# Optimization experiments

Measured on AMD Instinct MI355X. Metric: run time of the kernel, lower is better.

Reference implementation:

```python
import jax, jax.numpy as jnp
import numpy as np
from jax import lax

B, L = 4, 2048
D_MODEL, D_STATE, D_CONV, EXPAND = 1024, 16, 4, 2
D_INNER = EXPAND * D_MODEL          # 2048
DT_RANK = (D_MODEL + 15) // 16      # 64 (mamba_ssm 'auto')
EPS = 1e-5


def setup_inputs() -> dict:
    key = jax.random.key(0)
    ks = jax.random.split(key, 10)
    s = 0.02
    x = jax.random.normal(ks[0], (B, L, D_MODEL), dtype=jnp.float32)
    ln_w = jnp.ones((D_MODEL,), jnp.float32)
    ln_b = jnp.zeros((D_MODEL,), jnp.float32)
    W_in = jax.random.normal(ks[1], (2 * D_INNER, D_MODEL), jnp.float32) * s
    conv_w = jax.random.normal(ks[2], (D_INNER, 1, D_CONV), jnp.float32) * s
    conv_b = jnp.zeros((D_INNER,), jnp.float32)
    W_x = jax.random.normal(ks[3], (DT_RANK + 2 * D_STATE, D_INNER), jnp.float32) * s
    W_dt = jax.random.normal(ks[4], (D_INNER, DT_RANK), jnp.float32) * s
    b_dt = jax.random.uniform(ks[5], (D_INNER,), jnp.float32, -4.0, -2.0)  # softplus(b)~small dt
    A_log = jnp.log(jnp.tile(jnp.arange(1.0, D_STATE + 1.0, dtype=jnp.float32), (D_INNER, 1)))
    Dp = jnp.ones((D_INNER,), jnp.float32)
    W_out = jax.random.normal(ks[6], (D_MODEL, D_INNER), jnp.float32) * s
    return dict(x=x, ln_w=ln_w, ln_b=ln_b, W_in=W_in, conv_w=conv_w, conv_b=conv_b,
                W_x=W_x, W_dt=W_dt, b_dt=b_dt, A_log=A_log, Dp=Dp, W_out=W_out)


def _mamba_forward(x, ln_w, ln_b, W_in, conv_w, conv_b, W_x, W_dt, b_dt, A_log, Dp, W_out):
    # LayerNorm
    mu = jnp.mean(x, axis=-1, keepdims=True)
    var = jnp.mean(jnp.square(x - mu), axis=-1, keepdims=True)
    xn = (x - mu) * lax.rsqrt(var + EPS) * ln_w + ln_b

    # in_proj -> (x_in, z), each [B, L, D_INNER]
    xz = jnp.einsum('bld,ed->ble', xn, W_in)
    x_in, z = jnp.split(xz, 2, axis=-1)

    # depthwise causal conv1d over time + SiLU
    xt = jnp.transpose(x_in, (0, 2, 1))  # [B, D_INNER, L]
    xc = lax.conv_general_dilated(xt, conv_w, window_strides=(1,),
                                  padding=[(D_CONV - 1, 0)],
                                  feature_group_count=D_INNER)
    xc = jax.nn.silu(jnp.transpose(xc + conv_b[None, :, None], (0, 2, 1)))  # [B, L, D_INNER]

    # SSM parameterization
    x_dbl = jnp.einsum('bld,ed->ble', xc, W_x)  # [B, L, DT_RANK + 2*D_STATE]
    dt_r, Bs, Cs = jnp.split(x_dbl, [DT_RANK, DT_RANK + D_STATE], axis=-1)
    dt = jax.nn.softplus(jnp.einsum('blr,dr->bld', dt_r, W_dt) + b_dt)  # [B, L, D_INNER]
    A = -jnp.exp(A_log)  # [D_INNER, D_STATE]

    # selective scan over time (time-major)
    def step(h, inp):
        dt_t, B_t, C_t, u_t = inp  # [B,dI], [B,dS], [B,dS], [B,dI]
        dA = jnp.exp(dt_t[:, :, None] * A)                     # [B, dI, dS]
        h = dA * h + (dt_t * u_t)[:, :, None] * B_t[:, None, :]
        y = jnp.sum(h * C_t[:, None, :], axis=-1)              # [B, dI]
        return h, y

    h0 = jnp.zeros((B, D_INNER, D_STATE), x.dtype)
    xs = (jnp.swapaxes(dt, 0, 1), jnp.swapaxes(Bs, 0, 1),
          jnp.swapaxes(Cs, 0, 1), jnp.swapaxes(xc, 0, 1))
    _, ys = lax.scan(step, h0, xs)
    y = jnp.swapaxes(ys, 0, 1) + xc * Dp  # [B, L, D_INNER]

    # gate + out_proj + residual
    y = y * jax.nn.silu(z)
    out = jnp.einsum('ble,de->bld', y, W_out)
    return x + out


def reference(x, ln_w, ln_b, W_in, conv_w, conv_b, W_x, W_dt, b_dt, A_log, Dp, W_out):
    return _mamba_forward(x, ln_w, ln_b, W_in, conv_w, conv_b, W_x, W_dt, b_dt, A_log, Dp, W_out)
```

## Files before the change

kernel.cpp:

```cpp
#include <hip/hip_runtime.h>
#include <math.h>

#define BB 4
#define LL 2048
#define DM 1024
#define DI 2048
#define DS 16
#define DTR 64
#define TCH 256
#define TT 16

typedef unsigned short bf16;
typedef __attribute__((ext_vector_type(8))) short bf16x8;
typedef __attribute__((ext_vector_type(4))) float f32x4;
typedef __attribute__((ext_vector_type(2))) float f32x2;

__device__ inline float b2f(bf16 u) { return __uint_as_float(((unsigned)u) << 16); }
__device__ inline bf16 f2b(float f) {
    unsigned u = __float_as_uint(f);
    u += 0x7FFF + ((u >> 16) & 1);
    return (bf16)(u >> 16);
}

__device__ inline float4 ld4(const float* p) { return *(const float4*)p; }
__device__ inline float4 ld4(const bf16* p) {
    ushort4 v = *(const ushort4*)p;
    return make_float4(b2f(v.x), b2f(v.y), b2f(v.z), b2f(v.w));
}
__device__ inline void st1(float* p, float v) { *p = v; }
__device__ inline void st1(bf16* p, float v) { *p = f2b(v); }

__device__ inline float softplus_fast(float v) {
    return (v > 15.f) ? v : __logf(1.f + __expf(v));
}

__device__ inline void gld_lds16(const void* g, void* l) {
    __builtin_amdgcn_global_load_lds(
        (const __attribute__((address_space(1))) unsigned int*)g,
        (__attribute__((address_space(3))) unsigned int*)l, 16, 0, 0);
}

__device__ inline void dA2_tree(float c1, f32x2* dA2) {
    float c2 = c1 * c1;
    float c4 = c2 * c2;
    float c8 = c4 * c4;
    f32x2 c2v = {c2, c2};
    f32x2 c8v = {c8, c8};
    dA2[0] = (f32x2){c1, c2};
    dA2[1] = dA2[0] * c2v;
    dA2[2] = dA2[1] * c2v;
    dA2[3] = dA2[2] * c2v;
    dA2[4] = dA2[0] * c8v;
    dA2[5] = dA2[1] * c8v;
    dA2[6] = dA2[2] * c8v;
    dA2[7] = dA2[3] * c8v;
}

__global__ __launch_bounds__(256) void f2b_kernel(const float* __restrict__ in,
    bf16* __restrict__ out, int n4)
{
    int i = blockIdx.x * 256 + threadIdx.x;
    if (i >= n4) return;
    float4 v = *(const float4*)(in + (size_t)i * 4);
    ushort4 o = { f2b(v.x), f2b(v.y), f2b(v.z), f2b(v.w) };
    *(ushort4*)(out + (size_t)i * 4) = o;
}

__global__ __launch_bounds__(256) void prep_kernel(
    const float* __restrict__ x, const float* __restrict__ lw,
    const float* __restrict__ lb, bf16* __restrict__ xn,
    const float* __restrict__ W_in, bf16* __restrict__ W_in_b,
    const float* __restrict__ W_x, bf16* __restrict__ W_x_b,
    const float* __restrict__ W_dt, bf16* __restrict__ W_dt_b,
    const float* __restrict__ cw, bf16* __restrict__ cwt,
    const float* __restrict__ W_out, bf16* __restrict__ W_out_b,
    int dofast, int dowout)
{
    int blk = blockIdx.x;
    int tid = threadIdx.x;
    if (blk < BB * LL) {
        int row = blk;
        const float* xr = x + (size_t)row * DM;
        float4 v = *(const float4*)(xr + tid * 4);
        float s1 = v.x + v.y + v.z + v.w;
        float s2 = v.x * v.x + v.y * v.y + v.z * v.z + v.w * v.w;
        #pragma unroll
        for (int o = 32; o > 0; o >>= 1) {
            s1 += __shfl_xor(s1, o);
            s2 += __shfl_xor(s2, o);
        }
        __shared__ float r1[4], r2[4];
        __shared__ float smu, srs;
        int wv = tid >> 6;
        if ((tid & 63) == 0) { r1[wv] = s1; r2[wv] = s2; }
        __syncthreads();
        if (tid == 0) {
            float t1 = r1[0] + r1[1] + r1[2] + r1[3];
            float t2 = r2[0] + r2[1] + r2[2] + r2[3];
            float mu = t1 * (1.0f / DM);
            float var = t2 * (1.0f / DM) - mu * mu;
            smu = mu;
            srs = rsqrtf(var + 1e-5f);
        }
        __syncthreads();
        float mu = smu, rs = srs;
        float4 wv4 = *(const float4*)(lw + tid * 4);
        float4 bv4 = *(const float4*)(lb + tid * 4);
        ushort4 o;
        o.x = f2b((v.x - mu) * rs * wv4.x + bv4.x);
        o.y = f2b((v.y - mu) * rs * wv4.y + bv4.y);
        o.z = f2b((v.z - mu) * rs * wv4.z + bv4.z);
        o.w = f2b((v.w - mu) * rs * wv4.w + bv4.w);
        *(ushort4*)(xn + (size_t)row * DM + tid * 4) = o;
        return;
    }
    blk -= BB * LL;
    if (blk < 4096) {
        int i = blk * 256 + tid;
        float4 v = *(const float4*)(W_in + (size_t)i * 4);
        ushort4 o = { f2b(v.x), f2b(v.y), f2b(v.z), f2b(v.w) };
        *(ushort4*)(W_in_b + (size_t)i * 4) = o;
        return;
    }
    blk -= 4096;
    if (!dofast) return;
    if (blk < 192) {
        int i = blk * 256 + tid;
        float4 v = *(const float4*)(W_x + (size_t)i * 4);
        ushort4 o = { f2b(v.x), f2b(v.y), f2b(v.z), f2b(v.w) };
        *(ushort4*)(W_x_b + (size_t)i * 4) = o;
        return;
    }
    blk -= 192;
    if (blk < 128) {
        int i = blk * 256 + tid;
        float4 v = *(const float4*)(W_dt + (size_t)i * 4);
        ushort4 o = { f2b(v.x), f2b(v.y), f2b(v.z), f2b(v.w) };
        *(ushort4*)(W_dt_b + (size_t)i * 4) = o;
        return;
    }
    blk -= 128;
    if (blk < 8) {
        int d = blk * 256 + tid;
        float4 w = *(const float4*)(cw + d * 4);
        cwt[0 * DI + d] = f2b(w.x);
        cwt[1 * DI + d] = f2b(w.y);
        cwt[2 * DI + d] = f2b(w.z);
        cwt[3 * DI + d] = f2b(w.w);
        return;
    }
    blk -= 8;
    if (dowout && blk < 2048) {
        int i = blk * 256 + tid;
        float4 v = *(const float4*)(W_out + (size_t)i * 4);
        ushort4 o = { f2b(v.x), f2b(v.y), f2b(v.z), f2b(v.w) };
        *(ushort4*)(W_out_b + (size_t)i * 4) = o;
    }
}

#define BARR  do { asm volatile("" ::: "memory"); __builtin_amdgcn_s_barrier(); \
                   asm volatile("" ::: "memory"); } while (0)
#define LGKM0 do { asm volatile("s_waitcnt lgkmcnt(0)" ::: "memory"); \
                   __builtin_amdgcn_sched_barrier(0); } while (0)
#define VMC4  asm volatile("s_waitcnt vmcnt(4)" ::: "memory")
#define VMC2  asm volatile("s_waitcnt vmcnt(2)" ::: "memory")
#define SCHED0 __builtin_amdgcn_sched_barrier(0)

template<int EPI, typename TC>
__global__ __launch_bounds__(512, 2) void gemm_8p(
    const bf16* __restrict__ A, int lda,
    const bf16* __restrict__ B, int ldb,
    TC* __restrict__ C, int ldc,
    int K, const float* __restrict__ aux, int nbn)
{
    __shared__ bf16 lds[65536];
    char* L = (char*)lds;
    const int tid = threadIdx.x;
    const int lane = tid & 63;
    const int w = tid >> 6;
    const int wm = w >> 2;
    const int wn = w & 3;

    int nwg = gridDim.x;
    int bid = blockIdx.x;
    int sb = bid;
    if ((nwg & 7) == 0) sb = (bid & 7) * (nwg >> 3) + (bid >> 3);
    const int m0 = (sb / nbn) * 256;
    const int n0 = (sb % nbn) * 256;

    const size_t lda2 = (size_t)lda * 2;
    const size_t ldb2 = (size_t)ldb * 2;
    const int l8 = lane >> 3;
    const int scol = ((lane & 7) ^ l8) << 4;
    const size_t offA = (size_t)(w * 8 + l8) * lda2 + scol;
    const size_t offB = (size_t)(w * 8 + l8) * ldb2 + scol;
    const char* Ab = (const char*)A + (size_t)m0 * lda2;
    const char* Bb = (const char*)B + (size_t)n0 * ldb2;

    const int fm = lane & 15, fq = lane >> 4;
    const int prow = fm * 128;
    const int px0 = (fq << 4) ^ ((fm & 7) << 4);
    const int px1 = (64 | (fq << 4)) ^ ((fm & 7) << 4);
    const char* Lar = L + wm * 16384 + prow;
    const char* Lbr = L + 65536 + (wn >> 1) * 16384 + (wn & 1) * 8192 + prow;

    f32x4 acc[8][4] = {};
    bf16x8 a_[2][2], b_[4][2];

#define ST_A(sbuf, hh, t) do { \
    const char* s_ = Ab + (size_t)(hh) * 128 * lda2 + (size_t)(t) * 128 + offA; \
    gld_lds16(s_,             L + (sbuf) * 32768 + (hh) * 16384 + w * 1024); \
    gld_lds16(s_ + 64 * lda2, L + (sbuf) * 32768 + (hh) * 16384 + 8192 + w * 1024); \
  } while (0)
#define ST_B(sbuf, hh, t) do { \
    const char* s_ = Bb + (size_t)(hh) * 128 * ldb2 + (size_t)(t) * 128 + offB; \
    gld_lds16(s_,             L + 65536 + (sbuf) * 32768 + (hh) * 16384 + w * 1024); \
    gld_lds16(s_ + 64 * ldb2, L + 65536 + (sbuf) * 32768 + (hh) * 16384 + 8192 + w * 1024); \
  } while (0)
#define DS_A1(rb, q, kh) do { \
    a_[0][kh] = *(const bf16x8*)(Lar + (rb) * 32768 + ((q) * 32 +  0) * 128 + ((kh) ? px1 : px0)); \
    a_[1][kh] = *(const bf16x8*)(Lar + (rb) * 32768 + ((q) * 32 + 16) * 128 + ((kh) ? px1 : px0)); \
  } while (0)
#define DS_Bh(rb, kh) do { \
    _Pragma("unroll") \
    for (int ni = 0; ni < 4; ni++) \
      b_[ni][kh] = *(const bf16x8*)(Lbr + (rb) * 32768 + ni * 2048 + ((kh) ? px1 : px0)); \
  } while (0)
#define MFMA_H(q, kh) do { \
    _Pragma("unroll") \
    for (int mi = 0; mi < 2; mi++) \
      _Pragma("unroll") \
      for (int ni = 0; ni < 4; ni++) \
        acc[(q)*2+mi][ni] = __builtin_amdgcn_mfma_f32_16x16x32_bf16( \
            a_[mi][kh], b_[ni][kh], acc[(q)*2+mi][ni], 0, 0, 0); \
  } while (0)
#define PHASE(rb, q, rb2, q2, STAGE, DOVMC) do { \
    STAGE; \
    if (DOVMC) VMC4; \
    BARR; LGKM0; \
    __builtin_amdgcn_s_setprio(1); \
    MFMA_H(q, 0); \
    __builtin_amdgcn_s_setprio(0); \
    DS_A1(rb2, q2, 0); \
    if ((q) == 3) DS_Bh(rb2, 0); \
    SCHED0; \
    __builtin_amdgcn_s_setprio(1); \
    MFMA_H(q, 1); \
    __builtin_amdgcn_s_setprio(0); \
    DS_A1(rb2, q2, 1); \
    if ((q) == 3) DS_Bh(rb2, 1); \
    BARR; \
  } while (0)

    const int NT = K >> 6;
    ST_B(0, 0, 0); ST_B(0, 1, 0);
    ST_A(0, 0, 0); ST_A(0, 1, 0);
    ST_B(1, 0, 1); ST_B(1, 1, 1);
    VMC4;
    BARR;
    DS_Bh(0, 0); DS_Bh(0, 1);
    DS_A1(0, 0, 0); DS_A1(0, 0, 1);

    for (int t0 = 0; t0 < NT; t0 += 2) {
        const int tA1 = t0 + 1;
        const int tN2 = (t0 + 2 < NT) ? t0 + 2 : NT - 1;
        const int tN3 = (t0 + 3 < NT) ? t0 + 3 : NT - 1;
        PHASE(0, 0, 0, 1, ST_A(1, 0, tA1), 0);
        PHASE(0, 1, 0, 2, ST_A(1, 1, tA1), 0);
        PHASE(0, 2, 0, 3, ST_B(0, 0, tN2), 0);
        PHASE(0, 3, 1, 0, ST_B(0, 1, tN2), 1);
        PHASE(1, 0, 1, 1, ST_A(0, 0, tN2), 0);
        PHASE(1, 1, 1, 2, ST_A(0, 1, tN2), 0);
        PHASE(1, 2, 1, 3, ST_B(1, 0, tN3), 0);
        PHASE(1, 3, 0, 0, ST_B(1, 1, tN3), 1);
    }
    asm volatile("s_waitcnt vmcnt(0)" ::: "memory");

    #pragma unroll
    for (int i = 0; i < 8; i++) {
        #pragma unroll
        for (int ni = 0; ni < 4; ni++) {
            int n = n0 + wn * 64 + ni * 16 + fm;
            #pragma unroll
            for (int r = 0; r < 4; r++) {
                int m = m0 + wm * 128 + i * 16 + fq * 4 + r;
                float v = acc[i][ni][r];
                if (EPI == 2) v += aux[(size_t)m * ldc + n];
                st1(&C[(size_t)m * ldc + n], v);
            }
        }
    }
#undef ST_A
#undef ST_B
#undef DS_A1
#undef DS_Bh
#undef MFMA_H
#undef PHASE
}

template<int EPI, typename TC>
__global__ __launch_bounds__(512, 2) void gemm_8p_n128(
    const bf16* __restrict__ A, int lda,
    const bf16* __restrict__ B, int ldb,
    TC* __restrict__ C, int ldc,
    int K, const float* __restrict__ aux, int nbn)
{
    __shared__ bf16 lds[49152];
    char* L = (char*)lds;
    const int tid = threadIdx.x;
// ... 35 lines not shown
  } while (0)
#define ST_B1(sbuf, hh, t) do { \
    const char* s_ = Bb + (size_t)(hh) * 64 * ldb2 + (size_t)(t) * 128 + offB; \
    gld_lds16(s_, L + 65536 + (sbuf) * 16384 + (hh) * 8192 + w * 1024); \
  } while (0)
#define DS_A1h(rb, q, kh) do { \
    a_[kh] = *(const bf16x8*)(Lar + (rb) * 32768 + ((q) * 16) * 128 + ((kh) ? px1 : px0)); \
  } while (0)
#define DS_Bh(rb, kh) do { \
    _Pragma("unroll") \
    for (int ni = 0; ni < 4; ni++) \
      b_[ni][kh] = *(const bf16x8*)(Lbr + (rb) * 16384 + ni * 2048 + ((kh) ? px1 : px0)); \
  } while (0)
#define MFMA_Hh(q, kh) do { \
    _Pragma("unroll") \
    for (int ni = 0; ni < 4; ni++) \
      acc[q][ni] = __builtin_amdgcn_mfma_f32_16x16x32_bf16( \
          a_[kh], b_[ni][kh], acc[q][ni], 0, 0, 0); \
  } while (0)
#define PHASE(rb, q, rb2, q2, STAGE, DOVMC) do { \
    STAGE; \
    if (DOVMC) VMC2; \
    BARR; LGKM0; \
    __builtin_amdgcn_s_setprio(1); \
    MFMA_Hh(q, 0); \
    __builtin_amdgcn_s_setprio(0); \
    DS_A1h(rb2, q2, 0); \
    if ((q) == 3) DS_Bh(rb2, 0); \
    SCHED0; \
    __builtin_amdgcn_s_setprio(1); \
    MFMA_Hh(q, 1); \
    __builtin_amdgcn_s_setprio(0); \
    DS_A1h(rb2, q2, 1); \
    if ((q) == 3) DS_Bh(rb2, 1); \
    BARR; \
  } while (0)

    const int NT = K >> 6;
    ST_B1(0, 0, 0); ST_B1(0, 1, 0);
    ST_A(0, 0, 0); ST_A(0, 1, 0);
    ST_B1(1, 0, 1); ST_B1(1, 1, 1);
    VMC2;
    BARR;
    DS_Bh(0, 0); DS_Bh(0, 1);
    DS_A1h(0, 0, 0); DS_A1h(0, 0, 1);

    for (int t0 = 0; t0 < NT; t0 += 2) {
        const int tA1 = t0 + 1;
        const int tN2 = (t0 + 2 < NT) ? t0 + 2 : NT - 1;
        const int tN3 = (t0 + 3 < NT) ? t0 + 3 : NT - 1;
        PHASE(0, 0, 0, 1, ST_A(1, 0, tA1), 0);
        PHASE(0, 1, 0, 2, ST_A(1, 1, tA1), 0);
        PHASE(0, 2, 0, 3, ST_B1(0, 0, tN2), 0);
        PHASE(0, 3, 1, 0, ST_B1(0, 1, tN2), 1);
        PHASE(1, 0, 1, 1, ST_A(0, 0, tN2), 0);
        PHASE(1, 1, 1, 2, ST_A(0, 1, tN2), 0);
        PHASE(1, 2, 1, 3, ST_B1(1, 0, tN3), 0);
        PHASE(1, 3, 0, 0, ST_B1(1, 1, tN3), 1);
    }
    asm volatile("s_waitcnt vmcnt(0)" ::: "memory");

    #pragma unroll
    for (int i = 0; i < 4; i++) {
        #pragma unroll
        for (int ni = 0; ni < 4; ni++) {
            int n = n0 + wn * 64 + ni * 16 + fm;
            #pragma unroll
            for (int r = 0; r < 4; r++) {
                int m = m0 + wm * 64 + i * 16 + fq * 4 + r;
                float v = acc[i][ni][r];
                if (EPI == 2) v += aux[(size_t)m * ldc + n];
                st1(&C[(size_t)m * ldc + n], v);
            }
        }
    }
#undef ST_A
#undef ST_B1
#undef DS_A1h
#undef DS_Bh
#undef MFMA_Hh
#undef PHASE
}

template<int EPI, typename TC>
__global__ __launch_bounds__(256) void gemm_mfma(
    const bf16* __restrict__ A, int lda,
    const bf16* __restrict__ B, int ldb,
    TC* __restrict__ C, int ldc,
    int K, const float* __restrict__ aux)
{
    __shared__ bf16 As[128 * 32];
    __shared__ bf16 Bs[128 * 32];
    const int tid = threadIdx.x;
    const int lane = tid & 63;
    const int w = tid >> 6;
    const int wm = w >> 1, wn = w & 1;
    const int m0 = blockIdx.y * 128, n0 = blockIdx.x * 128;

    const int srow = lane >> 2;
    const int schunk = (lane & 3) * 8;

    const int fm = lane & 15;
    const int fq = lane >> 4;

    f32x4 acc[4][4] = {};

    for (int kt = 0; kt < K; kt += 32) {
        #pragma unroll
        for (int i = 0; i < 2; i++) {
            int r0 = i * 64 + w * 16;
            gld_lds16(A + (size_t)(m0 + r0 + srow) * lda + kt + schunk, &As[r0 * 32]);
            gld_lds16(B + (size_t)(n0 + r0 + srow) * ldb + kt + schunk, &Bs[r0 * 32]);
        }
        __syncthreads();
        bf16x8 af[4], bfr[4];
        #pragma unroll
        for (int i = 0; i < 4; i++) {
            af[i]  = *(const bf16x8*)&As[(wm * 64 + i * 16 + fm) * 32 + fq * 8];
            bfr[i] = *(const bf16x8*)&Bs[(wn * 64 + i * 16 + fm) * 32 + fq * 8];
        }
        #pragma unroll
        for (int i = 0; i < 4; i++)
            #pragma unroll
            for (int j = 0; j < 4; j++)
                acc[i][j] = __builtin_amdgcn_mfma_f32_16x16x32_bf16(
                    af[i], bfr[j], acc[i][j], 0, 0, 0);
        __syncthreads();
    }

    #pragma unroll
    for (int i = 0; i < 4; i++) {
        #pragma unroll
        for (int r = 0; r < 4; r++) {
            int m = m0 + wm * 64 + i * 16 + fq * 4 + r;
            #pragma unroll
            for (int j = 0; j < 4; j++) {
                int n = n0 + wn * 64 + j * 16 + fm;
                float v = acc[i][j][r];
                if (EPI == 1) {
                    v = softplus_fast(v + aux[n]);
                } else if (EPI == 2) {
                    v += aux[(size_t)m * ldc + n];
                }
                st1(&C[(size_t)m * ldc + n], v);
            }
        }
    }
}

__global__ __launch_bounds__(256) void xproj_mfma(
    const bf16* __restrict__ A,
    const bf16* __restrict__ Bm,
    float* __restrict__ Cx,
    bf16* __restrict__ dtr)
{
    __shared__ bf16 As[32 * 32];
    __shared__ bf16 Bs[128 * 32];
    const int tid = threadIdx.x;
    const int lane = tid & 63;
    const int w = tid >> 6;
    const int wm = w >> 1, wn = w & 1;
    const int m0 = blockIdx.x * 32;
    const int srow = lane >> 2;
    const int schunk = (lane & 3) * 8;
    const int fm = lane & 15;
    const int fq = lane >> 4;
    f32x4 acc[3] = {};
    for (int kt = 0; kt < DI; kt += 32) {
        if (w < 2) {
            int r0 = w * 16;
            gld_lds16(A + (size_t)(m0 + r0 + srow) * DI + kt + schunk, &As[r0 * 32]);
        }
        {
            int r0 = w * 32;
            gld_lds16(Bm + (size_t)(r0 + srow) * DI + kt + schunk, &Bs[r0 * 32]);
            gld_lds16(Bm + (size_t)(r0 + 16 + srow) * DI + kt + schunk, &Bs[(r0 + 16) * 32]);
        }
        __syncthreads();
        bf16x8 af = *(const bf16x8*)&As[(wm * 16 + fm) * 32 + fq * 8];
        #pragma unroll
        for (int j = 0; j < 3; j++) {
            bf16x8 bf = *(const bf16x8*)&Bs[((wn * 3 + j) * 16 + fm) * 32 + fq * 8];
            acc[j] = __builtin_amdgcn_mfma_f32_16x16x32_bf16(af, bf, acc[j], 0, 0, 0);
        }
        __syncthreads();
    }
    #pragma unroll
    for (int j = 0; j < 3; j++) {
        int col = (wn * 3 + j) * 16 + fm;
        #pragma unroll
        for (int r = 0; r < 4; r++) {
            int m = m0 + wm * 16 + fq * 4 + r;
            float v = acc[j][r];
            Cx[(size_t)m * 96 + col] = v;
            if (col < 64) dtr[(size_t)m * 64 + col] = f2b(v);
        }
    }
}

template<int EPI, typename TA, typename TB, typename TC>
__global__ __launch_bounds__(256) void gemm_nt(
    const TA* __restrict__ A, int lda,
    const TB* __restrict__ B, int ldb,
    TC* __restrict__ C, int ldc,
    int M, int N, int K,
    const float* __restrict__ aux)
{
    __shared__ float As[16][64];
    __shared__ float Bs[16][64];
    int tid = threadIdx.x;
    int m0 = blockIdx.y * 64, n0 = blockIdx.x * 64;
    int lr = tid >> 2;
    int lc = (tid & 3) * 4;
    int tm = tid >> 4;
    int tn = tid & 15;
    float acc[4][4] = {};
    for (int kt = 0; kt < K; kt += 16) {
        float4 av = ld4(A + (size_t)(m0 + lr) * lda + kt + lc);
        float4 bv = make_float4(0.f, 0.f, 0.f, 0.f);
        if (n0 + lr < N)
            bv = ld4(B + (size_t)(n0 + lr) * ldb + kt + lc);
        As[lc + 0][lr] = av.x; As[lc + 1][lr] = av.y;
        As[lc + 2][lr] = av.z; As[lc + 3][lr] = av.w;
        Bs[lc + 0][lr] = bv.x; Bs[lc + 1][lr] = bv.y;
        Bs[lc + 2][lr] = bv.z; Bs[lc + 3][lr] = bv.w;
        __syncthreads();
        #pragma unroll
        for (int k = 0; k < 16; k++) {
            float4 a4 = *(const float4*)&As[k][tm * 4];
            float4 b4 = *(const float4*)&Bs[k][tn * 4];
            float am[4] = {a4.x, a4.y, a4.z, a4.w};
            float bn[4] = {b4.x, b4.y, b4.z, b4.w};
            #pragma unroll
            for (int i = 0; i < 4; i++)
                #pragma unroll
                for (int j = 0; j < 4; j++)
                    acc[i][j] = fmaf(am[i], bn[j], acc[i][j]);
        }
        __syncthreads();
    }
    #pragma unroll
    for (int i = 0; i < 4; i++) {
        int m = m0 + tm * 4 + i;
        #pragma unroll
        for (int j = 0; j < 4; j++) {
            int n = n0 + tn * 4 + j;
            if (n >= N) continue;
            float v = acc[i][j];
            if (EPI == 1) {
                v = softplus_fast(v + aux[n]);
            }
            st1(&C[(size_t)m * ldc + n], v);
        }
    }
}

__global__ __launch_bounds__(256) void conv_silu_kernel(
    const bf16* __restrict__ xz, const bf16* __restrict__ cwt,
    const float* __restrict__ cb, bf16* __restrict__ xc)
{
    int idx = blockIdx.x * 256 + threadIdx.x;
    int d8 = idx & (DI / 8 - 1);
    int bl = idx >> 8;
    int l = bl & (LL - 1);
    int d0 = d8 * 8;
    float4 b0 = *(const float4*)(cb + d0);
    float4 b1 = *(const float4*)(cb + d0 + 4);
    float acc[8] = {b0.x, b0.y, b0.z, b0.w, b1.x, b1.y, b1.z, b1.w};
    #pragma unroll
    for (int k = 0; k < 4; k++) {
        if (l - 3 + k < 0) continue;
        bf16x8 xv = *(const bf16x8*)(xz + (size_t)(bl - 3 + k) * (2 * DI) + d0);
        bf16x8 wv = *(const bf16x8*)(cwt + k * DI + d0);
        #pragma unroll
        for (int j = 0; j < 8; j++)
            acc[j] = fmaf(b2f((bf16)xv[j]), b2f((bf16)wv[j]), acc[j]);
    }
    bf16x8 o;
    #pragma unroll
    for (int j = 0; j < 8; j++)
        o[j] = (short)f2b(acc[j] / (1.f + __expf(-acc[j])));
    *(bf16x8*)(xc + (size_t)bl * DI + d0) = o;
}

template<int NCC>
__global__ __launch_bounds__(256) void scan_part1(
    const float* __restrict__ xdbl, const bf16* __restrict__ dty,
    const bf16* __restrict__ xc, const float* __restrict__ A_log,
    float* __restrict__ Pd, float* __restrict__ S)
{
    __shared__ bf16 sdt[TT][TCH];
    __shared__ bf16 su[TT][TCH];
    __shared__ alignas(16) float sBC[TT][32];
    __shared__ int sflag;
    const int CH = LL / NCC;
    int bid = blockIdx.x;
    int cg = bid & 7;
    int c  = (bid >> 3) & (NCC - 1);
    int b  = (bid >> 3) / NCC;
    int d0 = cg * TCH;
    int tid = threadIdx.x;
    int w = tid >> 6, l = tid & 63;
    int lrow = l >> 5, lcol = (l & 31) * 8;
    int brow = l >> 3, bcol = (l & 7) * 4;
    int d = d0 + tid;

    if (tid == 0) sflag = 0;
    float Ads[16];
    #pragma unroll
    for (int q = 0; q < 4; q++) {
        float4 a4 = *(const float4*)&A_log[(size_t)d * DS + q * 4];
        Ads[q*4+0] = -__expf(a4.x); Ads[q*4+1] = -__expf(a4.y);
        Ads[q*4+2] = -__expf(a4.z); Ads[q*4+3] = -__expf(a4.w);
    }
    const float A0 = Ads[0];
    int bad = 0;
    #pragma unroll
    for (int s = 1; s < 16; s++) {
        float tgt = (float)(s + 1) * A0;
        bad |= (fabsf(Ads[s] - tgt) > 1e-5f * fabsf(tgt) + 1e-30f) ? 1 : 0;
    }
    __syncthreads();
    if (bad) atomicOr(&sflag, 1);
    __syncthreads();
    const int structured = (sflag == 0);

    const size_t rowbase = (size_t)b * LL + c * CH;
    float dsum = 0.f;

    if (structured) {
        f32x2 h2[8] = {};
        for (int t0 = 0; t0 < CH; t0 += TT) {
            #pragma unroll
            for (int pp = 0; pp < 2; pp++) {
                int r0 = (pp * 4 + w) * 2;
                size_t grow = rowbase + t0 + r0 + lrow;
                gld_lds16(dty + grow * DI + d0 + lcol, &sdt[r0][0]);
                gld_lds16(xc  + grow * DI + d0 + lcol, &su[r0][0]);
            }
            if (w < 2)
                gld_lds16(xdbl + (rowbase + t0 + w * 8 + brow) * 96 + DTR + bcol,
                          &sBC[w * 8][0]);
            __syncthreads();
            #pragma unroll
            for (int t = 0; t < TT; t++) {
                float dtv = b2f(sdt[t][tid]);
                float uv  = b2f(su[t][tid]);
                float tmp = dtv * uv;
                dsum += dtv;
                float4 B0 = ((const float4*)&sBC[t][0])[0];
                float4 B1 = ((const float4*)&sBC[t][0])[1];
                float4 B2 = ((const float4*)&sBC[t][0])[2];
                float4 B3 = ((const float4*)&sBC[t][0])[3];
                f32x2 bv2[8] = {{B0.x,B0.y},{B0.z,B0.w},{B1.x,B1.y},{B1.z,B1.w},
                                {B2.x,B2.y},{B2.z,B2.w},{B3.x,B3.y},{B3.z,B3.w}};
                f32x2 dA2[8];
                dA2_tree(__expf(dtv * A0), dA2);
                f32x2 tmp2 = {tmp, tmp};
                #pragma unroll
                for (int i = 0; i < 8; i++)
                    h2[i] = dA2[i] * h2[i] + tmp2 * bv2[i];
            }
            __syncthreads();
        }
        size_t o = ((size_t)(b * NCC + c) * DI + d) * DS;
        Pd[(size_t)(b * NCC + c) * DI + d] = dsum;
        #pragma unroll
        for (int q = 0; q < 4; q++)
            *(float4*)&S[o + q*4] = make_float4(h2[q*2].x, h2[q*2].y,
                                                h2[q*2+1].x, h2[q*2+1].y);
    } else {
        float h[16];
        #pragma unroll
        for (int s = 0; s < 16; s++) h[s] = 0.f;
        for (int t0 = 0; t0 < CH; t0 += TT) {
            #pragma unroll
            for (int pp = 0; pp < 2; pp++) {
                int r0 = (pp * 4 + w) * 2;
                size_t grow = rowbase + t0 + r0 + lrow;
                gld_lds16(dty + grow * DI + d0 + lcol, &sdt[r0][0]);
                gld_lds16(xc  + grow * DI + d0 + lcol, &su[r0][0]);
            }
            if (w < 2)
                gld_lds16(xdbl + (rowbase + t0 + w * 8 + brow) * 96 + DTR + bcol,
                          &sBC[w * 8][0]);
            __syncthreads();
            for (int t = 0; t < TT; t++) {
                float dtv = b2f(sdt[t][tid]);
                float uv  = b2f(su[t][tid]);
                float tmp = dtv * uv;
                dsum += dtv;
                const float4* bc = (const float4*)&sBC[t][0];
                float4 B0 = bc[0], B1 = bc[1], B2 = bc[2], B3 = bc[3];
                float Bv[16] = {B0.x,B0.y,B0.z,B0.w, B1.x,B1.y,B1.z,B1.w,
                                B2.x,B2.y,B2.z,B2.w, B3.x,B3.y,B3.z,B3.w};
                #pragma unroll
                for (int s = 0; s < 16; s++) {
                    float dA = __expf(dtv * Ads[s]);
                    h[s] = dA * h[s] + tmp * Bv[s];
                }
            }
            __syncthreads();
        }
        size_t o = ((size_t)(b * NCC + c) * DI + d) * DS;
        Pd[(size_t)(b * NCC + c) * DI + d] = dsum;
        #pragma unroll
        for (int q = 0; q < 4; q++)
            *(float4*)&S[o + q*4] = make_float4(h[q*4], h[q*4+1], h[q*4+2], h[q*4+3]);
    }
}

template<int NCC>
__global__ __launch_bounds__(256) void scan_combine(
    const float* __restrict__ A_log, const float* __restrict__ Pd,
    float* __restrict__ S)
{
    int g = blockIdx.x * 256 + threadIdx.x;
    int b = g >> 15;
    int rem = g & 32767;
    int d = rem >> 4;
    float Ads = -__expf(A_log[rem]);
    float h = 0.f;
    #pragma unroll
    for (int c = 0; c < NCC; c++) {
        size_t os = ((size_t)(b * NCC + c) << 15) + rem;
        float p = __expf(Ads * Pd[(size_t)(b * NCC + c) * DI + d]);
        float sv = S[os];
        S[os] = h;
        h = p * h + sv;
    }
}

template<int NCC>
__global__ __launch_bounds__(256) void scan_part2(
    const float* __restrict__ xdbl, bf16* __restrict__ dty,
    const bf16* __restrict__ xc, const bf16* __restrict__ xz,
    const float* __restrict__ A_log, const float* __restrict__ Dp,
    const float* __restrict__ Hin)
{
    __shared__ bf16 sdt[TT][TCH];
    __shared__ bf16 su[TT][TCH];
    __shared__ bf16 sz[TT][TCH];
    __shared__ alignas(16) float sBC[TT][32];
    __shared__ int sflag;
    const int CH = LL / NCC;
    int bid = blockIdx.x;
    int cg = bid & 7;
    int c  = (bid >> 3) & (NCC - 1);
    int b  = (bid >> 3) / NCC;
    int d0 = cg * TCH;
    int tid = threadIdx.x;
    int w = tid >> 6, l = tid & 63;
    int lrow = l >> 5, lcol = (l & 31) * 8;
    int brow = l >> 3, bcol = (l & 7) * 4;
    int d = d0 + tid;

    if (tid == 0) sflag = 0;
    float Ads[16];
    #pragma unroll
    for (int q = 0; q < 4; q++) {
        float4 a4 = *(const float4*)&A_log[(size_t)d * DS + q * 4];
        Ads[q*4+0] = -__expf(a4.x); Ads[q*4+1] = -__expf(a4.y);
        Ads[q*4+2] = -__expf(a4.z); Ads[q*4+3] = -__expf(a4.w);
    }
    const float A0 = Ads[0];
    int bad = 0;
    #pragma unroll
    for (int s = 1; s < 16; s++) {
        float tgt = (float)(s + 1) * A0;
        bad |= (fabsf(Ads[s] - tgt) > 1e-5f * fabsf(tgt) + 1e-30f) ? 1 : 0;
    }
    __syncthreads();
    if (bad) atomicOr(&sflag, 1);
    __syncthreads();
    const int structured = (sflag == 0);

    float dpd = Dp[d];
    size_t ho = ((size_t)(b * NCC + c) * DI + d) * DS;
    const size_t rowbase = (size_t)b * LL + c * CH;

    if (structured) {
        f32x2 h2[8];
        #pragma unroll
        for (int q = 0; q < 4; q++) {
            float4 hv = *(const float4*)&Hin[ho + q*4];
            h2[q*2]   = (f32x2){hv.x, hv.y};
            h2[q*2+1] = (f32x2){hv.z, hv.w};
        }
        for (int t0 = 0; t0 < CH; t0 += TT) {
            #pragma unroll
            for (int pp = 0; pp < 2; pp++) {
                int r0 = (pp * 4 + w) * 2;
                size_t grow = rowbase + t0 + r0 + lrow;
                gld_lds16(dty + grow * DI + d0 + lcol, &sdt[r0][0]);
                gld_lds16(xc  + grow * DI + d0 + lcol, &su[r0][0]);
                gld_lds16(xz  + grow * (2 * DI) + DI + d0 + lcol, &sz[r0][0]);
            }
            if (w < 2)
                gld_lds16(xdbl + (rowbase + t0 + w * 8 + brow) * 96 + DTR + bcol,
                          &sBC[w * 8][0]);
            __syncthreads();
            #pragma unroll
            for (int t = 0; t < TT; t++) {
                float dtv = b2f(sdt[t][tid]);
                float uv  = b2f(su[t][tid]);
                float tmp = dtv * uv;
                const float4* bc = (const float4*)&sBC[t][0];
                float4 B0 = bc[0], B1 = bc[1], B2 = bc[2], B3 = bc[3];
                float4 C0 = bc[4], C1 = bc[5], C2 = bc[6], C3 = bc[7];
                f32x2 bv2[8] = {{B0.x,B0.y},{B0.z,B0.w},{B1.x,B1.y},{B1.z,B1.w},
                                {B2.x,B2.y},{B2.z,B2.w},{B3.x,B3.y},{B3.z,B3.w}};
                f32x2 cv2[8] = {{C0.x,C0.y},{C0.z,C0.w},{C1.x,C1.y},{C1.z,C1.w},
                                {C2.x,C2.y},{C2.z,C2.w},{C3.x,C3.y},{C3.z,C3.w}};
                f32x2 dA2[8];
                dA2_tree(__expf(dtv * A0), dA2);
                f32x2 tmp2 = {tmp, tmp};
                f32x2 y2 = {0.f, 0.f};
                #pragma unroll
                for (int i = 0; i < 8; i++) {
                    h2[i] = dA2[i] * h2[i] + tmp2 * bv2[i];
                    y2 = y2 + h2[i] * cv2[i];
                }
                float y = y2.x + y2.y;
                float zv = b2f(sz[t][tid]);
                float yo = (y + uv * dpd) * (zv / (1.f + __expf(-zv)));
                dty[(rowbase + t0 + t) * DI + d] = f2b(yo);
            }
            __syncthreads();
        }
    } else {
        float h[16];
        #pragma unroll
        for (int q = 0; q < 4; q++) {
            float4 hv = *(const float4*)&Hin[ho + q*4];
            h[q*4] = hv.x; h[q*4+1] = hv.y; h[q*4+2] = hv.z; h[q*4+3] = hv.w;
        }
        for (int t0 = 0; t0 < CH; t0 += TT) {
            #pragma unroll
            for (int pp = 0; pp < 2; pp++) {
                int r0 = (pp * 4 + w) * 2;
                size_t grow = rowbase + t0 + r0 + lrow;
                gld_lds16(dty + grow * DI + d0 + lcol, &sdt[r0][0]);
                gld_lds16(xc  + grow * DI + d0 + lcol, &su[r0][0]);
                gld_lds16(xz  + grow * (2 * DI) + DI + d0 + lcol, &sz[r0][0]);
            }
            if (w < 2)
                gld_lds16(xdbl + (rowbase + t0 + w * 8 + brow) * 96 + DTR + bcol,
                          &sBC[w * 8][0]);
            __syncthreads();
            for (int t = 0; t < TT; t++) {
                float dtv = b2f(sdt[t][tid]);
                float uv  = b2f(su[t][tid]);
                float tmp = dtv * uv;
                const float4* bc = (const float4*)&sBC[t][0];
                float4 B0 = bc[0], B1 = bc[1], B2 = bc[2], B3 = bc[3];
                float4 C0 = bc[4], C1 = bc[5], C2 = bc[6], C3 = bc[7];
                float Bv[16] = {B0.x,B0.y,B0.z,B0.w, B1.x,B1.y,B1.z,B1.w,
                                B2.x,B2.y,B2.z,B2.w, B3.x,B3.y,B3.z,B3.w};
                float Cv[16] = {C0.x,C0.y,C0.z,C0.w, C1.x,C1.y,C1.z,C1.w,
                                C2.x,C2.y,C2.z,C2.w, C3.x,C3.y,C3.z,C3.w};
                float y0 = 0.f, y1 = 0.f;
                #pragma unroll
                for (int s = 0; s < 16; s++) {
                    float dA = __expf(dtv * Ads[s]);
                    h[s] = dA * h[s] + tmp * Bv[s];
                    if (s & 1) y1 = fmaf(h[s], Cv[s], y1);
                    else       y0 = fmaf(h[s], Cv[s], y0);
                }
                float y = y0 + y1;
                float zv = b2f(sz[t][tid]);
                float yo = (y + uv * dpd) * (zv / (1.f + __expf(-zv)));
                dty[(rowbase + t0 + t) * DI + d] = f2b(yo);
            }
            __syncthreads();
        }
    }
}

__global__ __launch_bounds__(256) void scan_mono(
    const float* __restrict__ xdbl, bf16* __restrict__ dty,
    const bf16* __restrict__ xc, const bf16* __restrict__ xz,
    const float* __restrict__ A_log, const float* __restrict__ Dp)
{
    const int TC = 64;
    int b = blockIdx.x >> 7;
    int dblk = blockIdx.x & 127;
    int d0 = dblk * 16;
    int tid = threadIdx.x;
    int s = tid & 15;
    int dg = tid >> 4;
    int d = d0 + dg;
    float Ads = -__expf(A_log[(size_t)d * DS + s]);
    float h = 0.f;
    __shared__ float sdt[TC][16], su[TC][16], sB[TC][16], sC[TC][16], sy[TC][16];
    const size_t rowbase = (size_t)b * LL;
    int wi = tid >> 2;
    int wj = (tid & 3) * 4;
    float4 dpv = *(const float4*)(Dp + d0 + wj);
    for (int t0 = 0; t0 < LL; t0 += TC) {
        {
            size_t g = (rowbase + t0 + wi) * (size_t)DI + d0 + wj;
            *(float4*)&sdt[wi][wj] = ld4(dty + g);
            *(float4*)&su[wi][wj]  = ld4(xc + g);
        }
        #pragma unroll
        for (int r = 0; r < 4; r++) {
            int i = (tid >> 4) + r * 16;
            size_t g = (rowbase + t0 + i) * 96;
            sB[i][s] = xdbl[g + DTR + s];
            sC[i][s] = xdbl[g + DTR + DS + s];
        }
        __syncthreads();
        for (int i = 0; i < TC; i++) {
            float dtv = sdt[i][dg];
            float dA = __expf(dtv * Ads);
            h = dA * h + dtv * su[i][dg] * sB[i][s];
            float yp = h * sC[i][s];
            yp += __shfl_xor(yp, 1);
            yp += __shfl_xor(yp, 2);
            yp += __shfl_xor(yp, 4);
            yp += __shfl_xor(yp, 8);
            if (s == 0) sy[i][dg] = yp;
        }
        __syncthreads();
        {
            size_t g  = (rowbase + t0 + wi) * (size_t)DI + d0 + wj;
            size_t gz = (rowbase + t0 + wi) * (size_t)(2 * DI) + DI + d0 + wj;
            float4 zv = ld4(xz + gz);
            float4 yv = *(const float4*)&sy[wi][wj];
            float4 uv = *(const float4*)&su[wi][wj];
            ushort4 o;
            o.x = f2b((yv.x + uv.x * dpv.x) * (zv.x / (1.f + __expf(-zv.x))));
            o.y = f2b((yv.y + uv.y * dpv.y) * (zv.y / (1.f + __expf(-zv.y))));
            o.z = f2b((yv.z + uv.z * dpv.z) * (zv.z / (1.f + __expf(-zv.z))));
            o.w = f2b((yv.w + uv.w * dpv.w) * (zv.w / (1.f + __expf(-zv.w))));
            *(ushort4*)(dty + g) = o;
        }
        __syncthreads();
    }
}

__global__ __launch_bounds__(256) void conv_silu_slow(
    const bf16* __restrict__ xz, const float* __restrict__ cw,
    const float* __restrict__ cb, bf16* __restrict__ xc)
{
    int idx = blockIdx.x * 256 + threadIdx.x;
    int d4 = idx & (DI / 4 - 1);
    int bl = idx >> 9;
    int l = bl & (LL - 1);
    int d0 = d4 * 4;
    float4 bias = *(const float4*)(cb + d0);
    float acc[4] = {bias.x, bias.y, bias.z, bias.w};
    #pragma unroll
    for (int k = 0; k < 4; k++) {
        if (l - 3 + k < 0) continue;
        float4 xv = ld4(xz + (size_t)(bl - 3 + k) * (2 * DI) + d0);
        acc[0] = fmaf(xv.x, cw[(d0 + 0) * 4 + k], acc[0]);
        acc[1] = fmaf(xv.y, cw[(d0 + 1) * 4 + k], acc[1]);
        acc[2] = fmaf(xv.z, cw[(d0 + 2) * 4 + k], acc[2]);
        acc[3] = fmaf(xv.w, cw[(d0 + 3) * 4 + k], acc[3]);
    }
    ushort4 o;
    o.x = f2b(acc[0] / (1.f + __expf(-acc[0])));
    o.y = f2b(acc[1] / (1.f + __expf(-acc[1])));
    o.z = f2b(acc[2] / (1.f + __expf(-acc[2])));
    o.w = f2b(acc[3] / (1.f + __expf(-acc[3])));
    *(ushort4*)(xc + (size_t)bl * DI + d0) = o;
}

extern "C" void kernel_launch(void* const* d_in, const int* in_sizes, int n_in,
                              void* d_out, int out_size, void* d_ws, size_t ws_size,
                              hipStream_t stream)
{
    const float* x      = (const float*)d_in[0];
    const float* ln_w   = (const float*)d_in[1];
    const float* ln_b   = (const float*)d_in[2];
    const float* W_in   = (const float*)d_in[3];
    const float* conv_w = (const float*)d_in[4];
    const float* conv_b = (const float*)d_in[5];
    const float* W_x    = (const float*)d_in[6];
    const float* W_dt   = (const float*)d_in[7];
    const float* b_dt   = (const float*)d_in[8];
    const float* A_log  = (const float*)d_in[9];
    const float* Dp     = (const float*)d_in[10];
    const float* W_out  = (const float*)d_in[11];
    float* out = (float*)d_out;

    const size_t R = (size_t)BB * LL;

    bf16*  xz    = (bf16*)d_ws;
    bf16*  dty   = xz + R * 2 * DI;
    float* xdbl  = (float*)(dty + R * DI);
    float* Pbuf  = xdbl + R * 96;

    const size_t headB = (size_t)((char*)Pbuf - (char*)d_ws);
    const size_t tailB = (size_t)(128 * DI + DI * DTR + R * DTR + 4 * DI) * 2 + 64;
    const size_t pU = (size_t)BB * DI * 4;
    const size_t sU = (size_t)BB * DI * DS * 4;
    const int ncc = (ws_size >= headB + 32 * (pU + sU) + tailB) ? 32 : 16;

    float* Sbuf   = (float*)((char*)Pbuf + (size_t)ncc * pU);
    bf16*  W_x_b  = (bf16*)((char*)Sbuf + (size_t)ncc * sU);
    bf16*  W_dt_b = W_x_b + 128 * DI;
    bf16*  dtr    = W_dt_b + DI * DTR;
    bf16*  cwt    = dtr + R * DTR;
    bf16*  W_out_b2 = cwt + 4 * DI;
    const size_t ws_need = (size_t)((char*)(cwt + 4 * DI) - (char*)d_ws);
    const bool fast = ws_size >= ws_need;
    const size_t ws_need_w = (size_t)((char*)(W_out_b2 + (size_t)DM * DI) - (char*)d_ws);
    const int dowout = (fast && ws_size >= ws_need_w) ? 1 : 0;

    bf16*  W_in_b  = dty;
    bf16*  W_out_b = xz;

    bf16* xn = (bf16*)d_out;
    bf16* xc = (bf16*)d_out;

    {
        int nb = BB * LL + 4096;
        if (fast) nb += 192 + 128 + 8 + (dowout ? 2048 : 0);
        prep_kernel<<<nb, 256, 0, stream>>>(
            x, ln_w, ln_b, xn, W_in, W_in_b, W_x, W_x_b, W_dt, W_dt_b,
            conv_w, cwt, W_out, W_out_b2, fast ? 1 : 0, dowout);
    }

    for (int half = 0; half < 2; half++) {
        gemm_8p<0, bf16><<<dim3(16 * 16), 512, 0, stream>>>(
            xn + (size_t)half * 4096 * DM, DM, W_in_b, DM,
            xz + (size_t)half * 4096 * (2 * DI), 2 * DI, DM, nullptr, 16);
    }

    if (fast) {
        conv_silu_kernel<<<(int)(R * DI / 8 / 256), 256, 0, stream>>>(
            xz, cwt, conv_b, xc);
        xproj_mfma<<<(int)(R / 32), 256, 0, stream>>>(xc, W_x_b, xdbl, dtr);
        gemm_mfma<1, bf16><<<dim3(DI / 128, R / 128), 256, 0, stream>>>(
            dtr, DTR, W_dt_b, DTR, dty, DI, DTR, b_dt);
        if (ncc == 32) {
            scan_part1<32><<<BB * 32 * (DI / TCH), 256, 0, stream>>>(
                xdbl, dty, xc, A_log, Pbuf, Sbuf);
            scan_combine<32><<<BB * DI * DS / 256, 256, 0, stream>>>(
                A_log, Pbuf, Sbuf);
            scan_part2<32><<<BB * 32 * (DI / TCH), 256, 0, stream>>>(
                xdbl, dty, xc, xz, A_log, Dp, Sbuf);
        } else {
            scan_part1<16><<<BB * 16 * (DI / TCH), 256, 0, stream>>>(
                xdbl, dty, xc, A_log, Pbuf, Sbuf);
            scan_combine<16><<<BB * DI * DS / 256, 256, 0, stream>>>(
                A_log, Pbuf, Sbuf);
            scan_part2<16><<<BB * 16 * (DI / TCH), 256, 0, stream>>>(
                xdbl, dty, xc, xz, A_log, Dp, Sbuf);
        }
    } else {
        conv_silu_slow<<<(int)(R * DI / 4 / 256), 256, 0, stream>>>(
            xz, conv_w, conv_b, xc);
        gemm_nt<0><<<dim3(2, R / 64), 256, 0, stream>>>(
            xc, DI, W_x, DI, xdbl, 96, (int)R, 96, DI, nullptr);
        gemm_nt<1><<<dim3(DI / 64, R / 64), 256, 0, stream>>>(
            xdbl, 96, W_dt, DTR, dty, DI, (int)R, DI, DTR, b_dt);
        scan_mono<<<BB * (DI / 16), 256, 0, stream>>>(
            xdbl, dty, xc, xz, A_log, Dp);
    }

    const bf16* W_out_use = dowout ? (const bf16*)W_out_b2 : (const bf16*)W_out_b;
    if (!dowout)
        f2b_kernel<<<(DM * DI / 4) / 256, 256, 0, stream>>>(W_out, W_out_b, DM * DI / 4);

    gemm_8p_n128<2, float><<<dim3((int)(R / 256) * (DM / 128)), 512, 0, stream>>>(
        dty, DI, W_out_use, DI, out, DM, DI, x, DM / 128);
}
```

Baseline: 378.3 us.

## Split xz into separate x_in/z buffers and reuse dead workspace for scan state

The in_proj output is now written to two contiguous [R, DI] buffers instead of one interleaved [R, 2*DI] buffer, using two full-size GEMM launches in place of two half-batch launches. After the conv consumes x_in, that region is reused for the scan partial buffers and the bf16 W_out copy, so the 32-chunk scan is always used regardless of workspace size. The W_out conversion moves from the prep kernel into extra blocks of the xproj kernel. This aims to cut workspace pressure, give conv and scan_part2 unit-stride rows, and overlap the weight cast with the small xproj GEMM, at the cost of more aliasing whose lifetimes must stay correct.

```diff
diff --git a/kernel.cpp b/kernel.cpp
--- a/kernel.cpp
+++ b/kernel.cpp
@@ -9,6 +9,7 @@
 #define DTR 64
 #define TCH 256
 #define TT 16
+#define NCC 32
 
 typedef unsigned short bf16;
 typedef __attribute__((ext_vector_type(8))) short bf16x8;
@@ -73,8 +74,7 @@
     const float* __restrict__ W_x, bf16* __restrict__ W_x_b,
     const float* __restrict__ W_dt, bf16* __restrict__ W_dt_b,
     const float* __restrict__ cw, bf16* __restrict__ cwt,
-    const float* __restrict__ W_out, bf16* __restrict__ W_out_b,
-    int dofast, int dowout)
+    int dofast)
 {
     int blk = blockIdx.x;
     int tid = threadIdx.x;
@@ -147,14 +147,6 @@
         cwt[1 * DI + d] = f2b(w.y);
         cwt[2 * DI + d] = f2b(w.z);
         cwt[3 * DI + d] = f2b(w.w);
-        return;
-    }
-    blk -= 8;
-    if (dowout && blk < 2048) {
-        int i = blk * 256 + tid;
-        float4 v = *(const float4*)(W_out + (size_t)i * 4);
-        ushort4 o = { f2b(v.x), f2b(v.y), f2b(v.z), f2b(v.w) };
-        *(ushort4*)(W_out_b + (size_t)i * 4) = o;
     }
 }
 
@@ -496,11 +488,20 @@
     const bf16* __restrict__ A,
     const bf16* __restrict__ Bm,
     float* __restrict__ Cx,
-    bf16* __restrict__ dtr)
+    bf16* __restrict__ dtr,
+    const float* __restrict__ W_out, bf16* __restrict__ W_out_b, int dowout)
 {
     __shared__ bf16 As[32 * 32];
     __shared__ bf16 Bs[128 * 32];
     const int tid = threadIdx.x;
+    if (blockIdx.x >= (BB * LL) / 32) {
+        if (!dowout) return;
+        int i = (blockIdx.x - (BB * LL) / 32) * 256 + tid;
+        float4 v = *(const float4*)(W_out + (size_t)i * 4);
+        ushort4 o = { f2b(v.x), f2b(v.y), f2b(v.z), f2b(v.w) };
+        *(ushort4*)(W_out_b + (size_t)i * 4) = o;
+        return;
+    }
     const int lane = tid & 63;
     const int w = tid >> 6;
     const int wm = w >> 1, wn = w & 1;
@@ -600,7 +601,7 @@
 }
 
 __global__ __launch_bounds__(256) void conv_silu_kernel(
-    const bf16* __restrict__ xz, const bf16* __restrict__ cwt,
+    const bf16* __restrict__ xin, const bf16* __restrict__ cwt,
     const float* __restrict__ cb, bf16* __restrict__ xc)
 {
     int idx = blockIdx.x * 256 + threadIdx.x;
@@ -614,7 +615,7 @@
     #pragma unroll
     for (int k = 0; k < 4; k++) {
         if (l - 3 + k < 0) continue;
-        bf16x8 xv = *(const bf16x8*)(xz + (size_t)(bl - 3 + k) * (2 * DI) + d0);
+        bf16x8 xv = *(const bf16x8*)(xin + (size_t)(bl - 3 + k) * DI + d0);
         bf16x8 wv = *(const bf16x8*)(cwt + k * DI + d0);
         #pragma unroll
         for (int j = 0; j < 8; j++)
@@ -627,7 +628,7 @@
     *(bf16x8*)(xc + (size_t)bl * DI + d0) = o;
 }
 
-template<int NCC>
+template<int NC2>
 __global__ __launch_bounds__(256) void scan_part1(
     const float* __restrict__ xdbl, const bf16* __restrict__ dty,
     const bf16* __restrict__ xc, const float* __restrict__ A_log,
@@ -637,11 +638,11 @@
     __shared__ bf16 su[TT][TCH];
     __shared__ alignas(16) float sBC[TT][32];
     __shared__ int sflag;
-    const int CH = LL / NCC;
+    const int CH = LL / NC2;
     int bid = blockIdx.x;
     int cg = bid & 7;
-    int c  = (bid >> 3) & (NCC - 1);
-    int b  = (bid >> 3) / NCC;
+    int c  = (bid >> 3) & (NC2 - 1);
+    int b  = (bid >> 3) / NC2;
     int d0 = cg * TCH;
     int tid = threadIdx.x;
     int w = tid >> 6, l = tid & 63;
@@ -707,8 +708,8 @@
             }
             __syncthreads();
         }
-        size_t o = ((size_t)(b * NCC + c) * DI + d) * DS;
-        Pd[(size_t)(b * NCC + c) * DI + d] = dsum;
+        size_t o = ((size_t)(b * NC2 + c) * DI + d) * DS;
+        Pd[(size_t)(b * NC2 + c) * DI + d] = dsum;
         #pragma unroll
         for (int q = 0; q < 4; q++)
             *(float4*)&S[o + q*4] = make_float4(h2[q*2].x, h2[q*2].y,
@@ -746,15 +747,15 @@
             }
             __syncthreads();
         }
-        size_t o = ((size_t)(b * NCC + c) * DI + d) * DS;
-        Pd[(size_t)(b * NCC + c) * DI + d] = dsum;
+        size_t o = ((size_t)(b * NC2 + c) * DI + d) * DS;
+        Pd[(size_t)(b * NC2 + c) * DI + d] = dsum;
         #pragma unroll
         for (int q = 0; q < 4; q++)
             *(float4*)&S[o + q*4] = make_float4(h[q*4], h[q*4+1], h[q*4+2], h[q*4+3]);
     }
 }
 
-template<int NCC>
+template<int NC2>
 __global__ __launch_bounds__(256) void scan_combine(
     const float* __restrict__ A_log, const float* __restrict__ Pd,
     float* __restrict__ S)
@@ -766,19 +767,19 @@
     float Ads = -__expf(A_log[rem]);
     float h = 0.f;
     #pragma unroll
-    for (int c = 0; c < NCC; c++) {
-        size_t os = ((size_t)(b * NCC + c) << 15) + rem;
-        float p = __expf(Ads * Pd[(size_t)(b * NCC + c) * DI + d]);
+    for (int c = 0; c < NC2; c++) {
+        size_t os = ((size_t)(b * NC2 + c) << 15) + rem;
+        float p = __expf(Ads * Pd[(size_t)(b * NC2 + c) * DI + d]);
         float sv = S[os];
         S[os] = h;
         h = p * h + sv;
     }
 }
 
-template<int NCC>
+template<int NC2>
 __global__ __launch_bounds__(256) void scan_part2(
     const float* __restrict__ xdbl, bf16* __restrict__ dty,
-    const bf16* __restrict__ xc, const bf16* __restrict__ xz,
+    const bf16* __restrict__ xc, const bf16* __restrict__ z,
     const float* __restrict__ A_log, const float* __restrict__ Dp,
     const float* __restrict__ Hin)
 {
@@ -787,11 +788,11 @@
     __shared__ bf16 sz[TT][TCH];
     __shared__ alignas(16) float sBC[TT][32];
     __shared__ int sflag;
-    const int CH = LL / NCC;
+    const int CH = LL / NC2;
     int bid = blockIdx.x;
     int cg = bid & 7;
-    int c  = (bid >> 3) & (NCC - 1);
-    int b  = (bid >> 3) / NCC;
+    int c  = (bid >> 3) & (NC2 - 1);
+    int b  = (bid >> 3) / NC2;
     int d0 = cg * TCH;
     int tid = threadIdx.x;
     int w = tid >> 6, l = tid & 63;
@@ -820,7 +821,7 @@
     const int structured = (sflag == 0);
 
     float dpd = Dp[d];
-    size_t ho = ((size_t)(b * NCC + c) * DI + d) * DS;
+    size_t ho = ((size_t)(b * NC2 + c) * DI + d) * DS;
     const size_t rowbase = (size_t)b * LL + c * CH;
 
     if (structured) {
@@ -838,7 +839,7 @@
                 size_t grow = rowbase + t0 + r0 + lrow;
                 gld_lds16(dty + grow * DI + d0 + lcol, &sdt[r0][0]);
                 gld_lds16(xc  + grow * DI + d0 + lcol, &su[r0][0]);
-                gld_lds16(xz  + grow * (2 * DI) + DI + d0 + lcol, &sz[r0][0]);
+                gld_lds16(z   + grow * DI + d0 + lcol, &sz[r0][0]);
             }
             if (w < 2)
                 gld_lds16(xdbl + (rowbase + t0 + w * 8 + brow) * 96 + DTR + bcol,
@@ -886,7 +887,7 @@
                 size_t grow = rowbase + t0 + r0 + lrow;
                 gld_lds16(dty + grow * DI + d0 + lcol, &sdt[r0][0]);
                 gld_lds16(xc  + grow * DI + d0 + lcol, &su[r0][0]);
-                gld_lds16(xz  + grow * (2 * DI) + DI + d0 + lcol, &sz[r0][0]);
+                gld_lds16(z   + grow * DI + d0 + lcol, &sz[r0][0]);
             }
             if (w < 2)
                 gld_lds16(xdbl + (rowbase + t0 + w * 8 + brow) * 96 + DTR + bcol,
@@ -923,7 +924,7 @@
 
 __global__ __launch_bounds__(256) void scan_mono(
     const float* __restrict__ xdbl, bf16* __restrict__ dty,
-    const bf16* __restrict__ xc, const bf16* __restrict__ xz,
+    const bf16* __restrict__ xc, const bf16* __restrict__ z,
     const float* __restrict__ A_log, const float* __restrict__ Dp)
 {
     const int TC = 64;
@@ -969,8 +970,7 @@
         __syncthreads();
         {
             size_t g  = (rowbase + t0 + wi) * (size_t)DI + d0 + wj;
-            size_t gz = (rowbase + t0 + wi) * (size_t)(2 * DI) + DI + d0 + wj;
-            float4 zv = ld4(xz + gz);
+            float4 zv = ld4(z + g);
             float4 yv = *(const float4*)&sy[wi][wj];
             float4 uv = *(const float4*)&su[wi][wj];
             ushort4 o;
@@ -985,7 +985,7 @@
 }
 
 __global__ __launch_bounds__(256) void conv_silu_slow(
-    const bf16* __restrict__ xz, const float* __restrict__ cw,
+    const bf16* __restrict__ xin, const float* __restrict__ cw,
     const float* __restrict__ cb, bf16* __restrict__ xc)
 {
     int idx = blockIdx.x * 256 + threadIdx.x;
@@ -998,7 +998,7 @@
     #pragma unroll
     for (int k = 0; k < 4; k++) {
         if (l - 3 + k < 0) continue;
-        float4 xv = ld4(xz + (size_t)(bl - 3 + k) * (2 * DI) + d0);
+        float4 xv = ld4(xin + (size_t)(bl - 3 + k) * DI + d0);
         acc[0] = fmaf(xv.x, cw[(d0 + 0) * 4 + k], acc[0]);
         acc[1] = fmaf(xv.y, cw[(d0 + 1) * 4 + k], acc[1]);
         acc[2] = fmaf(xv.z, cw[(d0 + 2) * 4 + k], acc[2]);
@@ -1032,84 +1032,66 @@
 
     const size_t R = (size_t)BB * LL;
 
-    bf16*  xz    = (bf16*)d_ws;
-    bf16*  dty   = xz + R * 2 * DI;
+    bf16*  xin   = (bf16*)d_ws;
+    bf16*  z     = xin + R * DI;
+    bf16*  dty   = z + R * DI;
     float* xdbl  = (float*)(dty + R * DI);
-    float* Pbuf  = xdbl + R * 96;
-
-    const size_t headB = (size_t)((char*)Pbuf - (char*)d_ws);
-    const size_t tailB = (size_t)(128 * DI + DI * DTR + R * DTR + 4 * DI) * 2 + 64;
-    const size_t pU = (size_t)BB * DI * 4;
-    const size_t sU = (size_t)BB * DI * DS * 4;
-    const int ncc = (ws_size >= headB + 32 * (pU + sU) + tailB) ? 32 : 16;
-
-    float* Sbuf   = (float*)((char*)Pbuf + (size_t)ncc * pU);
-    bf16*  W_x_b  = (bf16*)((char*)Sbuf + (size_t)ncc * sU);
+    bf16*  W_x_b  = (bf16*)(xdbl + R * 96);
     bf16*  W_dt_b = W_x_b + 128 * DI;
     bf16*  dtr    = W_dt_b + DI * DTR;
     bf16*  cwt    = dtr + R * DTR;
-    bf16*  W_out_b2 = cwt + 4 * DI;
     const size_t ws_need = (size_t)((char*)(cwt + 4 * DI) - (char*)d_ws);
     const bool fast = ws_size >= ws_need;
-    const size_t ws_need_w = (size_t)((char*)(W_out_b2 + (size_t)DM * DI) - (char*)d_ws);
-    const int dowout = (fast && ws_size >= ws_need_w) ? 1 : 0;
+
+    float* Pbuf  = (float*)xin;
+    float* Sbuf  = Pbuf + (size_t)BB * NCC * DI;
+    bf16*  W_out_b2 = (bf16*)(Sbuf + (size_t)BB * NCC * DI * DS);
 
     bf16*  W_in_b  = dty;
-    bf16*  W_out_b = xz;
+    bf16*  W_out_b = z;
 
     bf16* xn = (bf16*)d_out;
     bf16* xc = (bf16*)d_out;
 
     {
         int nb = BB * LL + 4096;
-        if (fast) nb += 192 + 128 + 8 + (dowout ? 2048 : 0);
+        if (fast) nb += 192 + 128 + 8;
         prep_kernel<<<nb, 256, 0, stream>>>(
             x, ln_w, ln_b, xn, W_in, W_in_b, W_x, W_x_b, W_dt, W_dt_b,
-            conv_w, cwt, W_out, W_out_b2, fast ? 1 : 0, dowout);
-    }
-
-    for (int half = 0; half < 2; half++) {
-        gemm_8p<0, bf16><<<dim3(16 * 16), 512, 0, stream>>>(
-            xn + (size_t)half * 4096 * DM, DM, W_in_b, DM,
-            xz + (size_t)half * 4096 * (2 * DI), 2 * DI, DM, nullptr, 16);
-    }
+            conv_w, cwt, fast ? 1 : 0);
+    }
+
+    gemm_8p<0, bf16><<<dim3((int)(R / 256) * (DI / 256)), 512, 0, stream>>>(
+        xn, DM, W_in_b, DM, xin, DI, DM, nullptr, DI / 256);
+    gemm_8p<0, bf16><<<dim3((int)(R / 256) * (DI / 256)), 512, 0, stream>>>(
+        xn, DM, W_in_b + (size_t)DI * DM, DM, z, DI, DM, nullptr, DI / 256);
 
     if (fast) {
         conv_silu_kernel<<<(int)(R * DI / 8 / 256), 256, 0, stream>>>(
-            xz, cwt, conv_b, xc);
-        xproj_mfma<<<(int)(R / 32), 256, 0, stream>>>(xc, W_x_b, xdbl, dtr);
+            xin, cwt, conv_b, xc);
+        xproj_mfma<<<(int)(R / 32) + 2048, 256, 0, stream>>>(
+            xc, W_x_b, xdbl, dtr, W_out, W_out_b2, 1);
         gemm_mfma<1, bf16><<<dim3(DI / 128, R / 128), 256, 0, stream>>>(
             dtr, DTR, W_dt_b, DTR, dty, DI, DTR, b_dt);
-        if (ncc == 32) {
-            scan_part1<32><<<BB * 32 * (DI / TCH), 256, 0, stream>>>(
-                xdbl, dty, xc, A_log, Pbuf, Sbuf);
-            scan_combine<32><<<BB * DI * DS / 256, 256, 0, stream>>>(
-                A_log, Pbuf, Sbuf);
-            scan_part2<32><<<BB * 32 * (DI / TCH), 256, 0, stream>>>(
-                xdbl, dty, xc, xz, A_log, Dp, Sbuf);
-        } else {
-            scan_part1<16><<<BB * 16 * (DI / TCH), 256, 0, stream>>>(
-                xdbl, dty, xc, A_log, Pbuf, Sbuf);
-            scan_combine<16><<<BB * DI * DS / 256, 256, 0, stream>>>(
-                A_log, Pbuf, Sbuf);
-            scan_part2<16><<<BB * 16 * (DI / TCH), 256, 0, stream>>>(
-                xdbl, dty, xc, xz, A_log, Dp, Sbuf);
-        }
+        scan_part1<NCC><<<BB * NCC * (DI / TCH), 256, 0, stream>>>(
+            xdbl, dty, xc, A_log, Pbuf, Sbuf);
+        scan_combine<NCC><<<BB * DI * DS / 256, 256, 0, stream>>>(
+            A_log, Pbuf, Sbuf);
+        scan_part2<NCC><<<BB * NCC * (DI / TCH), 256, 0, stream>>>(
+            xdbl, dty, xc, z, A_log, Dp, Sbuf);
+        gemm_8p_n128<2, float><<<dim3((int)(R / 256) * (DM / 128)), 512, 0, stream>>>(
+            dty, DI, W_out_b2, DI, out, DM, DI, x, DM / 128);
     } else {
         conv_silu_slow<<<(int)(R * DI / 4 / 256), 256, 0, stream>>>(
-            xz, conv_w, conv_b, xc);
+            xin, conv_w, conv_b, xc);
         gemm_nt<0><<<dim3(2, R / 64), 256, 0, stream>>>(
             xc, DI, W_x, DI, xdbl, 96, (int)R, 96, DI, nullptr);
         gemm_nt<1><<<dim3(DI / 64, R / 64), 256, 0, stream>>>(
             xdbl, 96, W_dt, DTR, dty, DI, (int)R, DI, DTR, b_dt);
         scan_mono<<<BB * (DI / 16), 256, 0, stream>>>(
-            xdbl, dty, xc, xz, A_log, Dp);
-    }
-
-    const bf16* W_out_use = dowout ? (const bf16*)W_out_b2 : (const bf16*)W_out_b;
-    if (!dowout)
+            xdbl, dty, xc, z, A_log, Dp);
         f2b_kernel<<<(DM * DI / 4) / 256, 256, 0, stream>>>(W_out, W_out_b, DM * DI / 4);
-
-    gemm_8p_n128<2, float><<<dim3((int)(R / 256) * (DM / 128)), 512, 0, stream>>>(
-        dty, DI, W_out_use, DI, out, DM, DI, x, DM / 128);
-}
+        gemm_8p_n128<2, float><<<dim3((int)(R / 256) * (DM / 128)), 512, 0, stream>>>(
+            dty, DI, W_out_b, DI, out, DM, DI, x, DM / 128);
+    }
+}
```

Result: slower. 390.0 us (+3.1%).
